# Optimization experiments

Hardware: AMD Instinct MI355X
Metric: run time of the kernel (lower is better)

Reference implementation:

```python
import jax, jax.numpy as jnp
import numpy as np

NUM_EXPERTS = 8
TOP_K = 2
ENTROPY_WEIGHT = 0.1
MAX_USAGE_RATIO = 0.3


def setup_inputs() -> dict:
    key = jax.random.key(0)
    k0, k1, k2 = jax.random.split(key, 3)
    B, S, D, H, E = 4, 4096, 1024, 1024, NUM_EXPERTS
    x = jax.random.normal(k0, (B, S, D), jnp.float32)
    gate_w = jax.random.normal(k1, (D, E), jnp.float32) * (1.0 / np.sqrt(D))
    gate_b = jnp.zeros((E,), jnp.float32)
    expert_w = jax.random.normal(k2, (E, D, H), jnp.float32) * (1.0 / np.sqrt(D))
    expert_b = jnp.zeros((E, H), jnp.float32)
    return {"x": x, "gate_w": gate_w, "gate_b": gate_b,
            "expert_w": expert_w, "expert_b": expert_b}


def reference(x, gate_w, gate_b, expert_w, expert_b):
    # x: [B, S, D]; dropout omitted (eval mode / deterministic reference)
    B, S, D = x.shape
    E = gate_w.shape[1]
    H = expert_w.shape[2]
    N = B * S
    xf = x.reshape(N, D)

    gate_logits = xf @ gate_w + gate_b            # [N, E]
    gate_probs = jax.nn.softmax(gate_logits, axis=-1)
    entropy = -jnp.sum(gate_probs * jnp.log(gate_probs + 1e-10), axis=-1).mean()
    entropy_loss = ENTROPY_WEIGHT * entropy

    topk_probs, topk_idx = jax.lax.top_k(gate_probs, TOP_K)   # [N, K]
    onehot = jax.nn.one_hot(topk_idx, E, dtype=xf.dtype)       # [N, K, E]
    combine = jnp.einsum('nk,nke->ne', topk_probs, onehot)     # [N, E] gating weight per expert

    # Weighted combine of per-expert Linear outputs; loop over small fixed E.
    out = jnp.zeros((N, H), xf.dtype)
    for e in range(E):
        out = out + combine[:, e:e + 1] * (xf @ expert_w[e] + expert_b[e])

    counts = jnp.sum(onehot, axis=(0, 1))                      # [E] tokens routed per expert
    usage_ratios = counts / N
    overuse_penalty = jnp.sum(jax.nn.relu(usage_ratios - MAX_USAGE_RATIO))

    return out.reshape(B, S, H), entropy_loss + overuse_penalty
```

## Files before the change

### kernel.cpp

```cpp
#include <hip/hip_runtime.h>
#include <hip/hip_bf16.h>

typedef __bf16 bf16x8 __attribute__((ext_vector_type(8)));
typedef __bf16 bf16x4 __attribute__((ext_vector_type(4)));
typedef float  f32x4  __attribute__((ext_vector_type(4)));

#define NTOK 16384
#define DDIM 1024
#define HDIM 1024
#define CNT_STRIDE 16

#define XB_OFF   0u
#define WT_OFF   33554432u
#define IDXP_OFF 50331648u
#define PPP_OFF  50397184u
#define TPID_OFF 50528256u
#define TPP_OFF  50593792u
#define CNT_OFF  50724864u
#define CUR_OFF  50728960u
#define BASE_OFF 50733056u
#define TILT_OFF 50733312u
#define NT_OFF   50736384u
#define ENT_OFF  50736388u
#define ZERO_LEN 11536u

typedef __attribute__((address_space(1))) void gvoid_t;
typedef __attribute__((address_space(3))) void lvoid_t;

__device__ __forceinline__ void cp16(void* lds, const void* g) {
  __builtin_amdgcn_global_load_lds((gvoid_t*)g, (lvoid_t*)lds, 16, 0, 0);
}

__global__ __launch_bounds__(256) void transpose_w(const float* __restrict__ w,
                                                   __bf16* __restrict__ wT) {
  const int b  = blockIdx.x;
  const int e  = b >> 8;
  const int d0 = ((b >> 4) & 15) * 64;
  const int h0 = (b & 15) * 64;
  __shared__ float tile[64][68];
  const int t = threadIdx.x;
  const float* base = w + ((size_t)e * DDIM + d0) * HDIM + h0;
#pragma unroll
  for (int it = 0; it < 4; ++it) {
    int dl = it * 16 + (t >> 4);
    int hl = (t & 15) * 4;
    float4 v = *(const float4*)(base + (size_t)dl * HDIM + hl);
    tile[dl][hl]     = v.x;
    tile[dl][hl + 1] = v.y;
    tile[dl][hl + 2] = v.z;
    tile[dl][hl + 3] = v.w;
  }
  __syncthreads();
  __bf16* obase = wT + ((size_t)e * HDIM + h0) * DDIM + d0;
#pragma unroll
  for (int it = 0; it < 4; ++it) {
    int hl = it * 16 + (t >> 4);
    int dl = (t & 15) * 4;
    bf16x4 bv;
    bv[0] = (__bf16)tile[dl][hl];
    bv[1] = (__bf16)tile[dl + 1][hl];
    bv[2] = (__bf16)tile[dl + 2][hl];
    bv[3] = (__bf16)tile[dl + 3][hl];
    *(bf16x4*)(obase + (size_t)hl * DDIM + dl) = bv;
  }
}

__global__ __launch_bounds__(256) void gate_kernel(
    const float* __restrict__ x, const float* __restrict__ gw,
    const float* __restrict__ gb, __bf16* __restrict__ xb,
    int* __restrict__ tt_pid, float2* __restrict__ tt_pp,
    int* __restrict__ cnt_g, float* __restrict__ ent_g) {
  __shared__ float gwT[8 * 1024];
  __shared__ int   lcnt[64];
  __shared__ float went[4];
  const int tid = threadIdx.x, w = tid >> 6, lane = tid & 63;
  for (int i = tid; i < 64; i += 256) lcnt[i] = 0;
#pragma unroll
  for (int i = 0; i < 32; ++i) {
    int lin = i * 256 + tid;
    gwT[(lin & 7) * 1024 + (lin >> 3)] = gw[lin];
  }
  __syncthreads();
  float4 gr[4][8];
#pragma unroll
  for (int j = 0; j < 4; ++j)
#pragma unroll
    for (int e = 0; e < 8; ++e)
      gr[j][e] = *(const float4*)&gwT[e * 1024 + j * 256 + lane * 4];
  float gbr[8];
#pragma unroll
  for (int e = 0; e < 8; ++e) gbr[e] = gb[e];

  float entacc = 0.f;
  for (int t = 0; t < 4; ++t) {
    const int n = blockIdx.x * 16 + w * 4 + t;
    float acc[8] = {0.f, 0.f, 0.f, 0.f, 0.f, 0.f, 0.f, 0.f};
#pragma unroll
    for (int j = 0; j < 4; ++j) {
      float4 v = *(const float4*)(x + (size_t)n * DDIM + j * 256 + lane * 4);
      bf16x4 bv;
      bv[0] = (__bf16)v.x; bv[1] = (__bf16)v.y;
      bv[2] = (__bf16)v.z; bv[3] = (__bf16)v.w;
      *(bf16x4*)(xb + (size_t)n * DDIM + j * 256 + lane * 4) = bv;
#pragma unroll
      for (int e = 0; e < 8; ++e) {
        float4 g = gr[j][e];
        acc[e] += v.x * g.x + v.y * g.y + v.z * g.z + v.w * g.w;
      }
    }
#pragma unroll
    for (int e = 0; e < 8; ++e) {
      float s = acc[e];
#pragma unroll
      for (int off = 1; off < 64; off <<= 1) s += __shfl_xor(s, off);
      acc[e] = s;
    }
    float p[8];
    float mx = -1e30f;
#pragma unroll
    for (int e = 0; e < 8; ++e) { p[e] = acc[e] + gbr[e]; mx = fmaxf(mx, p[e]); }
    float s = 0.f;
#pragma unroll
    for (int e = 0; e < 8; ++e) { p[e] = expf(p[e] - mx); s += p[e]; }
    float inv = 1.0f / s;
    float ent = 0.f;
#pragma unroll
    for (int e = 0; e < 8; ++e) { p[e] *= inv; ent -= p[e] * logf(p[e] + 1e-10f); }
    entacc += ent;
    int e1 = 0; float p1 = p[0];
#pragma unroll
    for (int e = 1; e < 8; ++e) if (p[e] > p1) { p1 = p[e]; e1 = e; }
    int e2 = (e1 == 0) ? 1 : 0; float p2 = p[e2];
#pragma unroll
    for (int e = 0; e < 8; ++e) if (e != e1 && p[e] > p2) { p2 = p[e]; e2 = e; }
    int   elo = (e1 < e2) ? e1 : e2;
    int   ehi = (e1 < e2) ? e2 : e1;
    float plo = (e1 < e2) ? p1 : p2;
    float phi = (e1 < e2) ? p2 : p1;
    int pid = elo * 8 + ehi;
    if (lane == 0) {
      tt_pid[n] = pid;
      tt_pp[n]  = make_float2(plo, phi);
      atomicAdd(&lcnt[pid], 1);
    }
  }
  if (lane == 0) went[w] = entacc;
  __syncthreads();
  if (tid < 64 && lcnt[tid]) atomicAdd(&cnt_g[tid * CNT_STRIDE], lcnt[tid]);
  if (tid == 0)
    atomicAdd(ent_g, went[0] + went[1] + went[2] + went[3]);
}

__global__ void scan_kernel(const int* __restrict__ cnt_g, int* __restrict__ base_g,
                            int4* __restrict__ tilt, int* __restrict__ nt_g,
                            const float* __restrict__ ent_g, float* __restrict__ loss_out) {
  if (threadIdx.x == 0) {
    int b = 0, t = 0;
    int ecnt[8] = {0, 0, 0, 0, 0, 0, 0, 0};
    for (int pid = 0; pid < 64; ++pid) {
      int c = cnt_g[pid * CNT_STRIDE];
      base_g[pid] = b;
      if (c > 0) {
        ecnt[pid >> 3] += c;
        ecnt[pid & 7]  += c;
        for (int r = 0; r < c; r += 128) tilt[t++] = make_int4(pid, r, c, b);
        b += c;
      }
    }
    *nt_g = t;
    float pen = 0.f;
    for (int e = 0; e < 8; ++e) {
      float r = (float)ecnt[e] / (float)NTOK - 0.3f;
      if (r > 0.f) pen += r;
    }
    loss_out[0] = 0.1f * (ent_g[0] / (float)NTOK) + pen;
  }
}

__global__ __launch_bounds__(256) void scatter_kernel(
    const int* __restrict__ tt_pid, const float2* __restrict__ tt_pp,
    const int* __restrict__ base_g, int* __restrict__ cur_g,
    int* __restrict__ idx_p, float2* __restrict__ pp_p) {
  __shared__ int lcnt[64], lbase[64];
  const int tid = threadIdx.x;
  if (tid < 64) lcnt[tid] = 0;
  __syncthreads();
  const int n = blockIdx.x * 256 + tid;
  const int pid = tt_pid[n];
  int lofs = atomicAdd(&lcnt[pid], 1);
  __syncthreads();
  if (tid < 64 && lcnt[tid]) lbase[tid] = atomicAdd(&cur_g[tid * CNT_STRIDE], lcnt[tid]);
  __syncthreads();
  int dst = base_g[pid] + lbase[pid] + lofs;
  idx_p[dst] = n;
  pp_p[dst]  = tt_pp[n];
}

__global__ __launch_bounds__(256) void moe_gemm(
    const __bf16* __restrict__ xb, const __bf16* __restrict__ wT,
    const float* __restrict__ eb, const int* __restrict__ idx_p,
    const float2* __restrict__ pp_p, const int4* __restrict__ tilt,
    const int* __restrict__ nt_g, float* __restrict__ out) {
  const int gy = blockIdx.y;
  if (gy >= *nt_g) return;
  const int4 te = tilt[gy];
  const int pid = te.x, row0 = te.y, cntp = te.z, gbase = te.w;
  const int elo = pid >> 3, ehi = pid & 7;
  const int gx = blockIdx.x;

  __shared__ __bf16 Ash[128 * 64];
  __shared__ __bf16 BloS[128 * 64];
  __shared__ __bf16 BhiS[128 * 64];
  __shared__ int    tok_s[128];
  __shared__ float2 pp_s[128];

  const int tid = threadIdx.x, w = tid >> 6, lane = tid & 63;
  if (tid < 128) {
    int s = row0 + tid;
    int g = gbase + ((s < cntp) ? s : (cntp - 1));
    tok_s[tid] = idx_p[g];
    pp_s[tid]  = pp_p[g];
  }
  __syncthreads();

  f32x4 accL[4][4], accH[4][4];
  const f32x4 zero = {0.f, 0.f, 0.f, 0.f};
#pragma unroll
  for (int mi = 0; mi < 4; ++mi)
#pragma unroll
    for (int ni = 0; ni < 4; ++ni) { accL[mi][ni] = zero; accH[mi][ni] = zero; }

  const int wm = (w >> 1) * 64, wn = (w & 1) * 64;
  const int tq = lane >> 4, tr = lane & 15, tr7 = tr & 7;
  const int rsub = lane >> 3;
  const int csw = ((lane & 7) ^ rsub) * 8;

  const __bf16* wlo = wT + (size_t)elo * HDIM * DDIM + (size_t)(gx * 128) * DDIM;
  const __bf16* whi = wT + (size_t)ehi * HDIM * DDIM + (size_t)(gx * 128) * DDIM;
  const __bf16* aptr[4];
  const __bf16* lptr[4];
  const __bf16* hptr[4];
#pragma unroll
  for (int it = 0; it < 4; ++it) {
    int r = it * 32 + w * 8 + rsub;
    aptr[it] = xb + (size_t)tok_s[r] * DDIM + csw;
    lptr[it] = wlo + (size_t)r * DDIM + csw;
    hptr[it] = whi + (size_t)r * DDIM + csw;
  }

  for (int kk = 0; kk < 16; ++kk) {
#pragma unroll
    for (int it = 0; it < 4; ++it) {
      const int rb = it * 32 + w * 8;
      cp16((char*)Ash  + rb * 128, aptr[it]); aptr[it] += 64;
      cp16((char*)BloS + rb * 128, lptr[it]); lptr[it] += 64;
      cp16((char*)BhiS + rb * 128, hptr[it]); hptr[it] += 64;
    }
    __syncthreads();
#pragma unroll
    for (int h = 0; h < 2; ++h) {
      const int co = (h << 2) | tq;
      bf16x8 a[4], bl[4], bh[4];
#pragma unroll
      for (int mi = 0; mi < 4; ++mi)
        a[mi] = *(const bf16x8*)((const char*)Ash + (wm + mi * 16 + tr) * 128 +
                                 ((co ^ tr7) << 4));
#pragma unroll
      for (int ni = 0; ni < 4; ++ni) {
        bl[ni] = *(const bf16x8*)((const char*)BloS + (wn + ni * 16 + tr) * 128 +
                                  ((co ^ tr7) << 4));
        bh[ni] = *(const bf16x8*)((const char*)BhiS + (wn + ni * 16 + tr) * 128 +
                                  ((co ^ tr7) << 4));
      }
#pragma unroll
      for (int mi = 0; mi < 4; ++mi)
#pragma unroll
        for (int ni = 0; ni < 4; ++ni) {
          accL[mi][ni] = __builtin_amdgcn_mfma_f32_16x16x32_bf16(a[mi], bl[ni], accL[mi][ni], 0, 0, 0);
          accH[mi][ni] = __builtin_amdgcn_mfma_f32_16x16x32_bf16(a[mi], bh[ni], accH[mi][ni], 0, 0, 0);
        }
    }
    __syncthreads();
  }

  float blov[4], bhiv[4];
#pragma unroll
  for (int ni = 0; ni < 4; ++ni) {
    int col = gx * 128 + wn + ni * 16 + tr;
    blov[ni] = eb[elo * HDIM + col];
    bhiv[ni] = eb[ehi * HDIM + col];
  }
#pragma unroll
  for (int mi = 0; mi < 4; ++mi)
#pragma unroll
    for (int r = 0; r < 4; ++r) {
      int lr = wm + mi * 16 + tq * 4 + r;
      if (row0 + lr < cntp) {
        int    tok = tok_s[lr];
        float2 pp  = pp_s[lr];
        float* orow = out + (size_t)tok * HDIM + gx * 128 + wn + tr;
#pragma unroll
        for (int ni = 0; ni < 4; ++ni)
          orow[ni * 16] = pp.x * (accL[mi][ni][r] + blov[ni]) +
                          pp.y * (accH[mi][ni][r] + bhiv[ni]);
      }
    }
}

extern "C" void kernel_launch(void* const* d_in, const int* in_sizes, int n_in,
                              void* d_out, int out_size, void* d_ws, size_t ws_size,
                              hipStream_t stream) {
  const float* x  = (const float*)d_in[0];
  const float* gw = (const float*)d_in[1];
  const float* gb = (const float*)d_in[2];
  const float* ew = (const float*)d_in[3];
  const float* eb = (const float*)d_in[4];
  float* out = (float*)d_out;
  char*  ws  = (char*)d_ws;

  __bf16* xb     = (__bf16*)(ws + XB_OFF);
  __bf16* wT     = (__bf16*)(ws + WT_OFF);
  int*    idx_p  = (int*)(ws + IDXP_OFF);
  float2* pp_p   = (float2*)(ws + PPP_OFF);
  int*    tt_pid = (int*)(ws + TPID_OFF);
  float2* tt_pp  = (float2*)(ws + TPP_OFF);
  int*    cnt_g  = (int*)(ws + CNT_OFF);
  int*    cur_g  = (int*)(ws + CUR_OFF);
  int*    base_g = (int*)(ws + BASE_OFF);
  int4*   tilt   = (int4*)(ws + TILT_OFF);
  int*    nt_g   = (int*)(ws + NT_OFF);
  float*  ent_g  = (float*)(ws + ENT_OFF);

  hipMemsetAsync(ws + CNT_OFF, 0, ZERO_LEN, stream);
  transpose_w<<<dim3(2048), 256, 0, stream>>>(ew, wT);
  gate_kernel<<<dim3(1024), 256, 0, stream>>>(x, gw, gb, xb, tt_pid, tt_pp,
                                              cnt_g, ent_g);
  scan_kernel<<<1, 64, 0, stream>>>(cnt_g, base_g, tilt, nt_g, ent_g,
                                    out + (size_t)NTOK * HDIM);
  scatter_kernel<<<dim3(64), 256, 0, stream>>>(tt_pid, tt_pp, base_g, cur_g,
                                               idx_p, pp_p);
  moe_gemm<<<dim3(8, 160), 256, 0, stream>>>(xb, wT, eb, idx_p, pp_p, tilt,
                                             nt_g, out);
}
```

Measured before the change: 327.9 us.

## Fuse prep kernels, merge scan into scatter, shrink GEMM N-tile for occupancy

The weight transpose and gate kernel become one launch that dispatches on block index, and the gate half now handles 2 tokens per wave over twice as many blocks, reading gate weights from LDS instead of registers. The single-thread scan kernel is folded into scatter: each block recomputes the prefix sums with a wave shuffle scan, and block 0 writes the tile list and the loss. The MoE GEMM N-tile drops from 128 to 64 columns with launch_bounds(256,4), doubling the grid and cutting LDS and accumulator registers to allow more resident waves. In exchange, each A tile is reloaded twice as often across the N dimension, and the scan work is repeated in every scatter block.

```diff
diff --git a/kernel.cpp b/kernel.cpp
--- a/kernel.cpp
+++ b/kernel.cpp
@@ -18,11 +18,10 @@
 #define TPP_OFF  50593792u
 #define CNT_OFF  50724864u
 #define CUR_OFF  50728960u
-#define BASE_OFF 50733056u
-#define TILT_OFF 50733312u
-#define NT_OFF   50736384u
-#define ENT_OFF  50736388u
-#define ZERO_LEN 11536u
+#define TILT_OFF 50733056u
+#define NT_OFF   50736128u
+#define ENT_OFF  50736132u
+#define ZERO_LEN 11280u
 
 typedef __attribute__((address_space(1))) void gvoid_t;
 typedef __attribute__((address_space(3))) void lvoid_t;
@@ -31,69 +30,73 @@
   __builtin_amdgcn_global_load_lds((gvoid_t*)g, (lvoid_t*)lds, 16, 0, 0);
 }
 
-__global__ __launch_bounds__(256) void transpose_w(const float* __restrict__ w,
-                                                   __bf16* __restrict__ wT) {
-  const int b  = blockIdx.x;
-  const int e  = b >> 8;
-  const int d0 = ((b >> 4) & 15) * 64;
-  const int h0 = (b & 15) * 64;
-  __shared__ float tile[64][68];
-  const int t = threadIdx.x;
-  const float* base = w + ((size_t)e * DDIM + d0) * HDIM + h0;
-#pragma unroll
-  for (int it = 0; it < 4; ++it) {
-    int dl = it * 16 + (t >> 4);
-    int hl = (t & 15) * 4;
-    float4 v = *(const float4*)(base + (size_t)dl * HDIM + hl);
-    tile[dl][hl]     = v.x;
-    tile[dl][hl + 1] = v.y;
-    tile[dl][hl + 2] = v.z;
-    tile[dl][hl + 3] = v.w;
-  }
-  __syncthreads();
-  __bf16* obase = wT + ((size_t)e * HDIM + h0) * DDIM + d0;
-#pragma unroll
-  for (int it = 0; it < 4; ++it) {
-    int hl = it * 16 + (t >> 4);
-    int dl = (t & 15) * 4;
-    bf16x4 bv;
-    bv[0] = (__bf16)tile[dl][hl];
-    bv[1] = (__bf16)tile[dl + 1][hl];
-    bv[2] = (__bf16)tile[dl + 2][hl];
-    bv[3] = (__bf16)tile[dl + 3][hl];
-    *(bf16x4*)(obase + (size_t)hl * DDIM + dl) = bv;
-  }
-}
-
-__global__ __launch_bounds__(256) void gate_kernel(
+union SmemU {
+  float tile[64][68];
+  struct {
+    float gwT[8 * 1024];
+    int   lcnt[64];
+    float went[4];
+  } g;
+};
+
+__global__ __launch_bounds__(256) void prep_kernel(
     const float* __restrict__ x, const float* __restrict__ gw,
-    const float* __restrict__ gb, __bf16* __restrict__ xb,
+    const float* __restrict__ gb, const float* __restrict__ ew,
+    __bf16* __restrict__ xb, __bf16* __restrict__ wT,
     int* __restrict__ tt_pid, float2* __restrict__ tt_pp,
     int* __restrict__ cnt_g, float* __restrict__ ent_g) {
-  __shared__ float gwT[8 * 1024];
-  __shared__ int   lcnt[64];
-  __shared__ float went[4];
-  const int tid = threadIdx.x, w = tid >> 6, lane = tid & 63;
-  for (int i = tid; i < 64; i += 256) lcnt[i] = 0;
+  __shared__ SmemU sm;
+  const int tid = threadIdx.x;
+
+  if (blockIdx.x < 2048) {
+    const int b  = blockIdx.x;
+    const int e  = b >> 8;
+    const int d0 = ((b >> 4) & 15) * 64;
+    const int h0 = (b & 15) * 64;
+    const float* base = ew + ((size_t)e * DDIM + d0) * HDIM + h0;
+#pragma unroll
+    for (int it = 0; it < 4; ++it) {
+      int dl = it * 16 + (tid >> 4);
+      int hl = (tid & 15) * 4;
+      float4 v = *(const float4*)(base + (size_t)dl * HDIM + hl);
+      sm.tile[dl][hl]     = v.x;
+      sm.tile[dl][hl + 1] = v.y;
+      sm.tile[dl][hl + 2] = v.z;
+      sm.tile[dl][hl + 3] = v.w;
+    }
+    __syncthreads();
+    __bf16* obase = wT + ((size_t)e * HDIM + h0) * DDIM + d0;
+#pragma unroll
+    for (int it = 0; it < 4; ++it) {
+      int hl = it * 16 + (tid >> 4);
+      int dl = (tid & 15) * 4;
+      bf16x4 bv;
+      bv[0] = (__bf16)sm.tile[dl][hl];
+      bv[1] = (__bf16)sm.tile[dl + 1][hl];
+      bv[2] = (__bf16)sm.tile[dl + 2][hl];
+      bv[3] = (__bf16)sm.tile[dl + 3][hl];
+      *(bf16x4*)(obase + (size_t)hl * DDIM + dl) = bv;
+    }
+    return;
+  }
+
+  const int gbid = blockIdx.x - 2048;
+  const int w = tid >> 6, lane = tid & 63;
+  if (tid < 64) sm.g.lcnt[tid] = 0;
 #pragma unroll
   for (int i = 0; i < 32; ++i) {
     int lin = i * 256 + tid;
-    gwT[(lin & 7) * 1024 + (lin >> 3)] = gw[lin];
-  }
-  __syncthreads();
-  float4 gr[4][8];
-#pragma unroll
-  for (int j = 0; j < 4; ++j)
-#pragma unroll
-    for (int e = 0; e < 8; ++e)
-      gr[j][e] = *(const float4*)&gwT[e * 1024 + j * 256 + lane * 4];
+    sm.g.gwT[(lin & 7) * 1024 + (lin >> 3)] = gw[lin];
+  }
   float gbr[8];
 #pragma unroll
   for (int e = 0; e < 8; ++e) gbr[e] = gb[e];
+  __syncthreads();
 
   float entacc = 0.f;
-  for (int t = 0; t < 4; ++t) {
-    const int n = blockIdx.x * 16 + w * 4 + t;
+#pragma unroll
+  for (int t = 0; t < 2; ++t) {
+    const int n = gbid * 8 + w * 2 + t;
     float acc[8] = {0.f, 0.f, 0.f, 0.f, 0.f, 0.f, 0.f, 0.f};
 #pragma unroll
     for (int j = 0; j < 4; ++j) {
@@ -104,7 +107,7 @@
       *(bf16x4*)(xb + (size_t)n * DDIM + j * 256 + lane * 4) = bv;
 #pragma unroll
       for (int e = 0; e < 8; ++e) {
-        float4 g = gr[j][e];
+        float4 g = *(const float4*)&sm.g.gwT[e * 1024 + j * 256 + lane * 4];
         acc[e] += v.x * g.x + v.y * g.y + v.z * g.z + v.w * g.w;
       }
     }
@@ -137,34 +140,50 @@
     int   ehi = (e1 < e2) ? e2 : e1;
     float plo = (e1 < e2) ? p1 : p2;
     float phi = (e1 < e2) ? p2 : p1;
-    int pid = elo * 8 + ehi;
     if (lane == 0) {
-      tt_pid[n] = pid;
+      tt_pid[n] = elo * 8 + ehi;
       tt_pp[n]  = make_float2(plo, phi);
-      atomicAdd(&lcnt[pid], 1);
-    }
-  }
-  if (lane == 0) went[w] = entacc;
-  __syncthreads();
-  if (tid < 64 && lcnt[tid]) atomicAdd(&cnt_g[tid * CNT_STRIDE], lcnt[tid]);
+      atomicAdd(&sm.g.lcnt[elo * 8 + ehi], 1);
+    }
+  }
+  if (lane == 0) sm.g.went[w] = entacc;
+  __syncthreads();
+  if (tid < 64 && sm.g.lcnt[tid]) atomicAdd(&cnt_g[tid * CNT_STRIDE], sm.g.lcnt[tid]);
   if (tid == 0)
-    atomicAdd(ent_g, went[0] + went[1] + went[2] + went[3]);
-}
-
-__global__ void scan_kernel(const int* __restrict__ cnt_g, int* __restrict__ base_g,
-                            int4* __restrict__ tilt, int* __restrict__ nt_g,
-                            const float* __restrict__ ent_g, float* __restrict__ loss_out) {
-  if (threadIdx.x == 0) {
-    int b = 0, t = 0;
+    atomicAdd(ent_g, sm.g.went[0] + sm.g.went[1] + sm.g.went[2] + sm.g.went[3]);
+}
+
+__global__ __launch_bounds__(256) void scatter_kernel(
+    const int* __restrict__ tt_pid, const float2* __restrict__ tt_pp,
+    const int* __restrict__ cnt_g, int* __restrict__ cur_g,
+    int* __restrict__ idx_p, float2* __restrict__ pp_p,
+    int4* __restrict__ tilt, int* __restrict__ nt_g,
+    const float* __restrict__ ent_g, float* __restrict__ loss_out) {
+  __shared__ int base_s[64], cnt_s[64], lcnt[64], lbase[64];
+  const int tid = threadIdx.x;
+  if (tid < 64) {
+    int c = cnt_g[tid * CNT_STRIDE];
+    cnt_s[tid] = c;
+    int v = c;
+#pragma unroll
+    for (int off = 1; off < 64; off <<= 1) {
+      int u = __shfl_up(v, off);
+      if ((tid & 63) >= off) v += u;
+    }
+    base_s[tid] = v - c;
+    lcnt[tid] = 0;
+  }
+  __syncthreads();
+  if (blockIdx.x == 0 && tid == 0) {
+    int t = 0;
     int ecnt[8] = {0, 0, 0, 0, 0, 0, 0, 0};
     for (int pid = 0; pid < 64; ++pid) {
-      int c = cnt_g[pid * CNT_STRIDE];
-      base_g[pid] = b;
+      int c = cnt_s[pid];
       if (c > 0) {
         ecnt[pid >> 3] += c;
         ecnt[pid & 7]  += c;
-        for (int r = 0; r < c; r += 128) tilt[t++] = make_int4(pid, r, c, b);
-        b += c;
+        for (int r = 0; r < c; r += 128)
+          tilt[t++] = make_int4(pid, r, c, base_s[pid]);
       }
     }
     *nt_g = t;
@@ -175,28 +194,18 @@
     }
     loss_out[0] = 0.1f * (ent_g[0] / (float)NTOK) + pen;
   }
-}
-
-__global__ __launch_bounds__(256) void scatter_kernel(
-    const int* __restrict__ tt_pid, const float2* __restrict__ tt_pp,
-    const int* __restrict__ base_g, int* __restrict__ cur_g,
-    int* __restrict__ idx_p, float2* __restrict__ pp_p) {
-  __shared__ int lcnt[64], lbase[64];
-  const int tid = threadIdx.x;
-  if (tid < 64) lcnt[tid] = 0;
-  __syncthreads();
   const int n = blockIdx.x * 256 + tid;
   const int pid = tt_pid[n];
   int lofs = atomicAdd(&lcnt[pid], 1);
   __syncthreads();
   if (tid < 64 && lcnt[tid]) lbase[tid] = atomicAdd(&cur_g[tid * CNT_STRIDE], lcnt[tid]);
   __syncthreads();
-  int dst = base_g[pid] + lbase[pid] + lofs;
+  int dst = base_s[pid] + lbase[pid] + lofs;
   idx_p[dst] = n;
   pp_p[dst]  = tt_pp[n];
 }
 
-__global__ __launch_bounds__(256) void moe_gemm(
+__global__ __launch_bounds__(256, 4) void moe_gemm(
     const __bf16* __restrict__ xb, const __bf16* __restrict__ wT,
     const float* __restrict__ eb, const int* __restrict__ idx_p,
     const float2* __restrict__ pp_p, const int4* __restrict__ tilt,
@@ -209,8 +218,8 @@
   const int gx = blockIdx.x;
 
   __shared__ __bf16 Ash[128 * 64];
-  __shared__ __bf16 BloS[128 * 64];
-  __shared__ __bf16 BhiS[128 * 64];
+  __shared__ __bf16 BloS[64 * 64];
+  __shared__ __bf16 BhiS[64 * 64];
   __shared__ int    tok_s[128];
   __shared__ float2 pp_s[128];
 
@@ -223,59 +232,58 @@
   }
   __syncthreads();
 
-  f32x4 accL[4][4], accH[4][4];
+  f32x4 accL[4][2], accH[4][2];
   const f32x4 zero = {0.f, 0.f, 0.f, 0.f};
 #pragma unroll
   for (int mi = 0; mi < 4; ++mi)
 #pragma unroll
-    for (int ni = 0; ni < 4; ++ni) { accL[mi][ni] = zero; accH[mi][ni] = zero; }
-
-  const int wm = (w >> 1) * 64, wn = (w & 1) * 64;
+    for (int ni = 0; ni < 2; ++ni) { accL[mi][ni] = zero; accH[mi][ni] = zero; }
+
+  const int wm = (w & 1) * 64, wn = (w >> 1) * 32;
   const int tq = lane >> 4, tr = lane & 15, tr7 = tr & 7;
   const int rsub = lane >> 3;
   const int csw = ((lane & 7) ^ rsub) * 8;
 
-  const __bf16* wlo = wT + (size_t)elo * HDIM * DDIM + (size_t)(gx * 128) * DDIM;
-  const __bf16* whi = wT + (size_t)ehi * HDIM * DDIM + (size_t)(gx * 128) * DDIM;
+  const __bf16* wlo = wT + (size_t)elo * HDIM * DDIM + (size_t)(gx * 64) * DDIM;
+  const __bf16* whi = wT + (size_t)ehi * HDIM * DDIM + (size_t)(gx * 64) * DDIM;
   const __bf16* aptr[4];
-  const __bf16* lptr[4];
-  const __bf16* hptr[4];
-#pragma unroll
-  for (int it = 0; it < 4; ++it) {
-    int r = it * 32 + w * 8 + rsub;
-    aptr[it] = xb + (size_t)tok_s[r] * DDIM + csw;
-    lptr[it] = wlo + (size_t)r * DDIM + csw;
-    hptr[it] = whi + (size_t)r * DDIM + csw;
-  }
+#pragma unroll
+  for (int it = 0; it < 4; ++it)
+    aptr[it] = xb + (size_t)tok_s[it * 32 + w * 8 + rsub] * DDIM + csw;
+  const __bf16* lptr = wlo + (size_t)(w * 8 + rsub) * DDIM + csw;
+  const __bf16* hptr = whi + (size_t)(w * 8 + rsub) * DDIM + csw;
 
   for (int kk = 0; kk < 16; ++kk) {
+    const int k0 = kk * 64;
 #pragma unroll
     for (int it = 0; it < 4; ++it) {
       const int rb = it * 32 + w * 8;
-      cp16((char*)Ash  + rb * 128, aptr[it]); aptr[it] += 64;
-      cp16((char*)BloS + rb * 128, lptr[it]); lptr[it] += 64;
-      cp16((char*)BhiS + rb * 128, hptr[it]); hptr[it] += 64;
+      cp16((char*)Ash + rb * 128, aptr[it]);
+      aptr[it] += 64;
+    }
+#pragma unroll
+    for (int it = 0; it < 2; ++it) {
+      const int rb = it * 32 + w * 8;
+      cp16((char*)BloS + rb * 128, lptr + (size_t)it * 32 * DDIM + k0);
+      cp16((char*)BhiS + rb * 128, hptr + (size_t)it * 32 * DDIM + k0);
     }
     __syncthreads();
 #pragma unroll
     for (int h = 0; h < 2; ++h) {
-      const int co = (h << 2) | tq;
-      bf16x8 a[4], bl[4], bh[4];
+      const int co = ((h << 2) | tq) ^ tr7;
+      bf16x8 a[4], bl[2], bh[2];
 #pragma unroll
       for (int mi = 0; mi < 4; ++mi)
-        a[mi] = *(const bf16x8*)((const char*)Ash + (wm + mi * 16 + tr) * 128 +
-                                 ((co ^ tr7) << 4));
-#pragma unroll
-      for (int ni = 0; ni < 4; ++ni) {
-        bl[ni] = *(const bf16x8*)((const char*)BloS + (wn + ni * 16 + tr) * 128 +
-                                  ((co ^ tr7) << 4));
-        bh[ni] = *(const bf16x8*)((const char*)BhiS + (wn + ni * 16 + tr) * 128 +
-                                  ((co ^ tr7) << 4));
+        a[mi] = *(const bf16x8*)((const char*)Ash + (wm + mi * 16 + tr) * 128 + (co << 4));
+#pragma unroll
+      for (int ni = 0; ni < 2; ++ni) {
+        bl[ni] = *(const bf16x8*)((const char*)BloS + (wn + ni * 16 + tr) * 128 + (co << 4));
+        bh[ni] = *(const bf16x8*)((const char*)BhiS + (wn + ni * 16 + tr) * 128 + (co << 4));
       }
 #pragma unroll
       for (int mi = 0; mi < 4; ++mi)
 #pragma unroll
-        for (int ni = 0; ni < 4; ++ni) {
+        for (int ni = 0; ni < 2; ++ni) {
           accL[mi][ni] = __builtin_amdgcn_mfma_f32_16x16x32_bf16(a[mi], bl[ni], accL[mi][ni], 0, 0, 0);
           accH[mi][ni] = __builtin_amdgcn_mfma_f32_16x16x32_bf16(a[mi], bh[ni], accH[mi][ni], 0, 0, 0);
         }
@@ -283,10 +291,10 @@
     __syncthreads();
   }
 
-  float blov[4], bhiv[4];
-#pragma unroll
-  for (int ni = 0; ni < 4; ++ni) {
-    int col = gx * 128 + wn + ni * 16 + tr;
+  float blov[2], bhiv[2];
+#pragma unroll
+  for (int ni = 0; ni < 2; ++ni) {
+    int col = gx * 64 + wn + ni * 16 + tr;
     blov[ni] = eb[elo * HDIM + col];
     bhiv[ni] = eb[ehi * HDIM + col];
   }
@@ -298,9 +306,9 @@
       if (row0 + lr < cntp) {
         int    tok = tok_s[lr];
         float2 pp  = pp_s[lr];
-        float* orow = out + (size_t)tok * HDIM + gx * 128 + wn + tr;
-#pragma unroll
-        for (int ni = 0; ni < 4; ++ni)
+        float* orow = out + (size_t)tok * HDIM + gx * 64 + wn + tr;
+#pragma unroll
+        for (int ni = 0; ni < 2; ++ni)
           orow[ni * 16] = pp.x * (accL[mi][ni][r] + blov[ni]) +
                           pp.y * (accH[mi][ni][r] + bhiv[ni]);
       }
@@ -326,19 +334,16 @@
   float2* tt_pp  = (float2*)(ws + TPP_OFF);
   int*    cnt_g  = (int*)(ws + CNT_OFF);
   int*    cur_g  = (int*)(ws + CUR_OFF);
-  int*    base_g = (int*)(ws + BASE_OFF);
   int4*   tilt   = (int4*)(ws + TILT_OFF);
   int*    nt_g   = (int*)(ws + NT_OFF);
   float*  ent_g  = (float*)(ws + ENT_OFF);
 
   hipMemsetAsync(ws + CNT_OFF, 0, ZERO_LEN, stream);
-  transpose_w<<<dim3(2048), 256, 0, stream>>>(ew, wT);
-  gate_kernel<<<dim3(1024), 256, 0, stream>>>(x, gw, gb, xb, tt_pid, tt_pp,
-                                              cnt_g, ent_g);
-  scan_kernel<<<1, 64, 0, stream>>>(cnt_g, base_g, tilt, nt_g, ent_g,
-                                    out + (size_t)NTOK * HDIM);
-  scatter_kernel<<<dim3(64), 256, 0, stream>>>(tt_pid, tt_pp, base_g, cur_g,
-                                               idx_p, pp_p);
-  moe_gemm<<<dim3(8, 160), 256, 0, stream>>>(xb, wT, eb, idx_p, pp_p, tilt,
-                                             nt_g, out);
-}
+  prep_kernel<<<dim3(4096), 256, 0, stream>>>(x, gw, gb, ew, xb, wT,
+                                              tt_pid, tt_pp, cnt_g, ent_g);
+  scatter_kernel<<<dim3(64), 256, 0, stream>>>(tt_pid, tt_pp, cnt_g, cur_g,
+                                               idx_p, pp_p, tilt, nt_g, ent_g,
+                                               out + (size_t)NTOK * HDIM);
+  moe_gemm<<<dim3(16, 160), 256, 0, stream>>>(xb, wT, eb, idx_p, pp_p, tilt,
+                                              nt_g, out);
+}
```

New measurement: 335.8 us. +2.4%, slower.
